# Kernel optimization log

Hardware: AMD Instinct MI355X
Metric: run time of the kernel (lower is better)

Reference implementation:

```python
import jax, jax.numpy as jnp
import numpy as np

N_HEADS, N_LEVELS, N_POINTS = 8, 3, 4


def _bilinear_sample(valf, Hl, Wl, grid):
    """torch.F.grid_sample(mode='bilinear', padding_mode='zeros', align_corners=False).
    valf: [B, nH, hd, Hl*Wl] flattened per-head value map
    grid: [B, Q, nH, P, 2] normalized (x, y) in [-1, 1]
    returns [B, nH, hd, Q, P]
    """
    B, Q, nH, P, _ = grid.shape
    hd = valf.shape[2]
    # unnormalize (align_corners=False)
    ix = ((grid[..., 0] + 1.0) * Wl - 1.0) * 0.5  # [B,Q,nH,P]
    iy = ((grid[..., 1] + 1.0) * Hl - 1.0) * 0.5
    x0 = jnp.floor(ix); y0 = jnp.floor(iy)
    x1 = x0 + 1.0;      y1 = y0 + 1.0
    # corner weights
    w00 = (x1 - ix) * (y1 - iy)
    w01 = (ix - x0) * (y1 - iy)
    w10 = (x1 - ix) * (iy - y0)
    w11 = (ix - x0) * (iy - y0)

    def gather(xi, yi):
        inb = (xi >= 0) & (xi <= Wl - 1) & (yi >= 0) & (yi <= Hl - 1)  # zero padding
        xc = jnp.clip(xi, 0, Wl - 1).astype(jnp.int32)
        yc = jnp.clip(yi, 0, Hl - 1).astype(jnp.int32)
        idx = yc * Wl + xc                              # [B,Q,nH,P]
        idx = idx.transpose(0, 2, 1, 3).reshape(B, nH, 1, Q * P)
        idx = jnp.broadcast_to(idx, (B, nH, hd, Q * P))
        g = jnp.take_along_axis(valf, idx, axis=3)      # [B,nH,hd,Q*P]
        g = g.reshape(B, nH, hd, Q, P)
        mask = inb.transpose(0, 2, 1, 3)[:, :, None, :, :]
        return g * mask

    def w_(w):  # [B,Q,nH,P] -> [B,nH,1,Q,P]
        return w.transpose(0, 2, 1, 3)[:, :, None, :, :]

    return (gather(x0, y0) * w_(w00) + gather(x1, y0) * w_(w01)
            + gather(x0, y1) * w_(w10) + gather(x1, y1) * w_(w11))


def _deform_attn(query, feats, reference_points,
                 W_off, b_off, W_attn, b_attn, W_val, b_val, W_out, b_out):
    B, Q, D = query.shape
    nH, L, P = N_HEADS, N_LEVELS, N_POINTS
    hd = D // nH
    # sampling offsets: tanh * 0.5
    off = jnp.tanh(query @ W_off + b_off).reshape(B, Q, nH, L, P, 2) * 0.5
    # attention weights: softmax over levels*points
    aw = jax.nn.softmax((query @ W_attn + b_attn).reshape(B, Q, nH, L * P), axis=-1)
    aw = aw.reshape(B, Q, nH, L, P)

    out = jnp.zeros((B, Q, nH, hd), dtype=query.dtype)
    for lvl, feat in enumerate(feats):
        Hl, Wl = feat.shape[2], feat.shape[3]
        # value projection on flattened map
        v = feat.reshape(B, D, Hl * Wl).transpose(0, 2, 1) @ W_val + b_val  # [B,S,D]
        valf = v.reshape(B, Hl * Wl, nH, hd).transpose(0, 2, 3, 1)          # [B,nH,hd,S]
        grid = (reference_points[:, :, None, None, :] + off[:, :, :, lvl]) * 2.0 - 1.0  # [B,Q,nH,P,2]
        sampled = _bilinear_sample(valf, Hl, Wl, grid)                      # [B,nH,hd,Q,P]
        w = aw[:, :, :, lvl].transpose(0, 2, 1, 3)[:, :, None, :, :]        # [B,nH,1,Q,P]
        out = out + (sampled * w).sum(-1).transpose(0, 3, 1, 2)             # [B,Q,nH,hd]
    return out.reshape(B, Q, D) @ W_out + b_out


def setup_inputs() -> dict:
    key = jax.random.key(0)
    ks = jax.random.split(key, 13)
    B, Q, D = 4, 8400, 256
    return {
        "query": jax.random.normal(ks[0], (B, Q, D), jnp.float32),
        "feat0": jax.random.normal(ks[1], (B, D, 80, 80), jnp.float32),
        "feat1": jax.random.normal(ks[2], (B, D, 40, 40), jnp.float32),
        "feat2": jax.random.normal(ks[3], (B, D, 20, 20), jnp.float32),
        "reference_points": jax.random.uniform(ks[4], (B, Q, 2), jnp.float32),
        "W_off": jax.random.normal(ks[5], (D, N_HEADS * N_LEVELS * N_POINTS * 2), jnp.float32) * 0.02,
        "b_off": jax.random.normal(ks[6], (N_HEADS * N_LEVELS * N_POINTS * 2,), jnp.float32) * 0.02,
        "W_attn": jax.random.normal(ks[7], (D, N_HEADS * N_LEVELS * N_POINTS), jnp.float32) * 0.02,
        "b_attn": jax.random.normal(ks[8], (N_HEADS * N_LEVELS * N_POINTS,), jnp.float32) * 0.02,
        "W_val": jax.random.normal(ks[9], (D, D), jnp.float32) * (1.0 / np.sqrt(D)),
        "b_val": jnp.zeros((D,), jnp.float32),
        "W_out": jax.random.normal(ks[10], (D, D), jnp.float32) * (1.0 / np.sqrt(D)),
        "b_out": jnp.zeros((D,), jnp.float32),
    }


def reference(query, feat0, feat1, feat2, reference_points,
              W_off, b_off, W_attn, b_attn, W_val, b_val, W_out, b_out):
    return _deform_attn(query, [feat0, feat1, feat2], reference_points,
                        W_off, b_off, W_attn, b_attn, W_val, b_val, W_out, b_out)
```

## Files before the change

kernel.cpp:

```cpp
#include <hip/hip_runtime.h>
#include <math.h>

#define NH    8
#define DIM   256
#define NQ    8400
#define BATCH 4
#define STOT  8400
#define MQ    (BATCH * NQ)

typedef _Float16 f16;
typedef __attribute__((ext_vector_type(2))) _Float16 f16x2;
typedef __attribute__((ext_vector_type(8))) _Float16 f16x8;
typedef __attribute__((ext_vector_type(8))) unsigned short u16x8;
typedef __attribute__((ext_vector_type(4))) float  f32x4;

static __device__ __forceinline__ void gl_lds16(const void* g, void* l) {
    __builtin_amdgcn_global_load_lds(
        (const __attribute__((address_space(1))) unsigned int*)g,
        (__attribute__((address_space(3))) unsigned int*)(unsigned int)(unsigned long long)l,
        16, 0, 0);
}

__global__ __launch_bounds__(256) void prep_all(
    const float* __restrict__ feat0, const float* __restrict__ feat1,
    const float* __restrict__ feat2, const float* __restrict__ query,
    const float* __restrict__ W_val, const float* __restrict__ W_out,
    const float* __restrict__ W_off, const float* __restrict__ W_attn,
    const float* __restrict__ b_off, const float* __restrict__ b_attn,
    f16* __restrict__ Af, f16* __restrict__ Qh,
    f16* __restrict__ Wvt, f16* __restrict__ Wot,
    f16* __restrict__ Wch, float* __restrict__ bcat)
{
    const int z = blockIdx.z;
    const int t = threadIdx.x;
    __shared__ float tile[32][33];
    const int c = t & 31, r = t >> 5;

    if (z == 5) {
        size_t base = ((size_t)(blockIdx.x * 8 + blockIdx.y) * 256 + t) * 16;
        if (base < (size_t)MQ * 256) {
            #pragma unroll
            for (int i = 0; i < 2; ++i) {
                float4 q0 = *(const float4*)(query + base + i * 8);
                float4 q1 = *(const float4*)(query + base + i * 8 + 4);
                f16x8 hv;
                hv[0] = (f16)q0.x; hv[1] = (f16)q0.y; hv[2] = (f16)q0.z; hv[3] = (f16)q0.w;
                hv[4] = (f16)q1.x; hv[5] = (f16)q1.y; hv[6] = (f16)q1.z; hv[7] = (f16)q1.w;
                *(f16x8*)(Qh + base + i * 8) = hv;
            }
        }
        return;
    }

    if (z == 4) {
        const int xb = blockIdx.x;
        if (xb > 25) return;
        if (xb == 25) {
            if (blockIdx.y == 0)
                for (int i = t; i < 288; i += 256)
                    bcat[i] = (i < 192) ? b_off[i] : b_attn[i - 192];
            return;
        }
        const float* W; f16* oH; int Nw, n0, nb;
        if (xb < 8)       { W = W_val;  oH = Wvt; Nw = 256; n0 = 0;   nb = xb * 32; }
        else if (xb < 16) { W = W_out;  oH = Wot; Nw = 256; n0 = 0;   nb = (xb - 8) * 32; }
        else if (xb < 22) { W = W_off;  oH = Wch; Nw = 192; n0 = 0;   nb = (xb - 16) * 32; }
        else              { W = W_attn; oH = Wch; Nw = 96;  n0 = 192; nb = (xb - 22) * 32; }
        const int k0 = blockIdx.y * 32;
        #pragma unroll
        for (int i = 0; i < 4; ++i) {
            int k = k0 + r + i * 8, n = nb + c;
            tile[r + i * 8][c] = (n < Nw) ? W[(size_t)k * Nw + n] : 0.f;
        }
        __syncthreads();
        #pragma unroll
        for (int i = 0; i < 4; ++i) {
            int n = nb + r + i * 8, k = k0 + c;
            if (n < Nw)
                oH[(size_t)(n0 + n) * 256 + k] = (f16)tile[c][r + i * 8];
        }
        return;
    }

    const int b = z;
    const int s0 = blockIdx.x * 32, k0 = blockIdx.y * 32;
    if (s0 >= 8400) return;
    const float* f0b = feat0 + (size_t)b * 256 * 6400;
    const float* f1b = feat1 + (size_t)b * 256 * 1600;
    const float* f2b = feat2 + (size_t)b * 256 * 400;
    #pragma unroll
    for (int i = 0; i < 4; ++i) {
        int rr = r + i * 8;
        int s = s0 + c;
        float v = 0.f;
        if (s < 8400) {
            const float* fp; int S, sl;
            if (s < 6400)      { fp = f0b; S = 6400; sl = s; }
            else if (s < 8000) { fp = f1b; S = 1600; sl = s - 6400; }
            else               { fp = f2b; S = 400;  sl = s - 8000; }
            v = fp[(size_t)(k0 + rr) * S + sl];
        }
        tile[rr][c] = v;
    }
    __syncthreads();
    #pragma unroll
    for (int i = 0; i < 4; ++i) {
        int s = s0 + r + i * 8, k = k0 + c;
        if (s < 8400)
            Af[((size_t)b * 8400 + s) * 256 + k] = (f16)tile[c][r + i * 8];
    }
}

template<int KIND>
__global__ __launch_bounds__(256) void gemm_glds(
    const f16* __restrict__ A0, const f16* __restrict__ A1,
    const f16* __restrict__ B0, const f16* __restrict__ B1,
    const float* __restrict__ bias0, const float* __restrict__ bias1,
    f16* __restrict__ valh, float* __restrict__ rawo, f16* __restrict__ attnh,
    float* __restrict__ Cf)
{
    __shared__ f16 Ah[128 * 32];
    __shared__ f16 Bs[128 * 32];

    const bool split = (KIND == 0) && (blockIdx.x >= 2);
    const int bn = split ? (blockIdx.x - 2) * 128 : blockIdx.x * 128;
    const int bm = blockIdx.y * 128;
    const int N = split ? 288 : 256;
    const f16* Ag = split ? A1 : A0;
    const f16* Bg = split ? B1 : B0;
    const float* bias = split ? bias1 : bias0;

    const int t = threadIdx.x;
    const int lane = t & 63, w = t >> 6;
    const int wm = (w & 1) * 64, wn = (w >> 1) * 64;
    const int l15 = lane & 15, quad = lane >> 4;

    const int fstage = ((t >> 2) & 3) ^ ((t >> 4) & 3);
    const int qs = (t & 3) ^ fstage;
    const int ffrag = (l15 & 3) ^ ((l15 >> 2) & 3);
    const int qf = quad ^ ffrag;

    f32x4 acc[4][4];
    #pragma unroll
    for (int i = 0; i < 4; ++i)
        #pragma unroll
        for (int j = 0; j < 4; ++j)
            acc[i][j] = (f32x4){0.f, 0.f, 0.f, 0.f};

    for (int k0 = 0; k0 < 256; k0 += 32) {
        #pragma unroll
        for (int i = 0; i < 2; ++i) {
            int row = i * 64 + (t >> 2);
            int slot = i * 256 + t;
            int gr = bm + row; if (gr > MQ - 1) gr = MQ - 1;
            gl_lds16(Ag + (size_t)gr * 256 + k0 + qs * 8, &Ah[slot * 8]);
            int gn = bn + row; if (gn > N - 1) gn = N - 1;
            gl_lds16(Bg + (size_t)gn * 256 + k0 + qs * 8, &Bs[slot * 8]);
        }
        __syncthreads();

        f16x8 af[4], bfv[4];
        #pragma unroll
        for (int mt = 0; mt < 4; ++mt)
            af[mt] = *(const f16x8*)&Ah[((wm + mt * 16 + l15) * 4 + qf) * 8];
        #pragma unroll
        for (int nt = 0; nt < 4; ++nt)
            bfv[nt] = *(const f16x8*)&Bs[((wn + nt * 16 + l15) * 4 + qf) * 8];
        #pragma unroll
        for (int mt = 0; mt < 4; ++mt)
            #pragma unroll
            for (int nt = 0; nt < 4; ++nt)
                acc[mt][nt] = __builtin_amdgcn_mfma_f32_16x16x32_f16(af[mt], bfv[nt], acc[mt][nt], 0, 0, 0);
        __syncthreads();
    }

    #pragma unroll
    for (int nt = 0; nt < 4; ++nt) {
        int col = bn + wn + nt * 16 + l15;
        float bv = (col < N) ? bias[col] : 0.f;
        #pragma unroll
        for (int mt = 0; mt < 4; ++mt) {
            int row0 = bm + wm + mt * 16 + quad * 4;
            #pragma unroll
            for (int r = 0; r < 4; ++r) {
                int row = row0 + r;
                if (row >= MQ || col >= N) continue;
                float v = acc[mt][nt][r] + bv;
                if (KIND == 1) {
                    Cf[(size_t)row * 256 + col] = v;
                } else if (!split) {
                    int bb = row / STOT, s = row - bb * STOT;
                    int h = col >> 5, c = col & 31;
                    valh[(((size_t)(bb * 8 + h)) * STOT + s) * 32 + c] = (f16)v;
                } else if (col < 192) {
                    rawo[(size_t)row * 192 + col] = v;
                } else {
                    attnh[(size_t)row * 96 + (col - 192)] = (f16)v;
                }
            }
        }
    }
}

__global__ __launch_bounds__(256) void sample_v6(
    const f16* __restrict__ valh,
    const float* __restrict__ raw_off,
    const f16* __restrict__ attnh,
    const float* __restrict__ refp,
    f16* __restrict__ out_h)
{
    const int bx = blockIdx.x;
    const int xcd = bx & 7;
    const int b = xcd >> 1;
    const int qi = (bx >> 3) * 2 + (xcd & 1);
    const int bq0 = b * NQ + qi * 8;
    const int t = threadIdx.x;

    __shared__ int      s_idx[8][96][4];
    __shared__ unsigned s_wp[8][96][4];
    __shared__ float    s_m[8][8];
    __shared__ float    s_inv[8][8];

    if (t < 64) {
        int q = t >> 3, h = t & 7;
        const f16* a = attnh + (size_t)(bq0 + q) * 96 + h * 12;
        float m = (float)a[0];
        #pragma unroll
        for (int j = 1; j < 12; ++j) m = fmaxf(m, (float)a[j]);
        float s = 0.f;
        #pragma unroll
        for (int j = 0; j < 12; ++j) s += expf((float)a[j] - m);
        s_m[q][h] = m;
        s_inv[q][h] = 1.f / s;
    }
    __syncthreads();

    for (int i = t; i < 768; i += 256) {
        int q = i / 96, p = i - q * 96;
        int h = p / 12, lp = p - h * 12, l = lp >> 2;
        const int dims[3]   = {80, 40, 20};
        const int bases_[3] = {0, 6400, 8000};
        int Wl = dims[l], base = bases_[l];
        float logit = (float)attnh[(size_t)(bq0 + q) * 96 + p];
        float aw = expf(logit - s_m[q][h]) * s_inv[q][h];
        size_t ro = (size_t)(bq0 + q) * 192 + h * 24 + lp * 2;
        float rawx = raw_off[ro], rawy = raw_off[ro + 1];
        float rx = refp[(size_t)(bq0 + q) * 2];
        float ry = refp[(size_t)(bq0 + q) * 2 + 1];
        float ix = (rx + tanhf(rawx) * 0.5f) * Wl - 0.5f;
        float iy = (ry + tanhf(rawy) * 0.5f) * Wl - 0.5f;
        float x0f = floorf(ix), y0f = floorf(iy);
        float fx = ix - x0f, fy = iy - y0f;
        int x0 = (int)x0f, y0 = (int)y0f;
        float w00 = (1.f - fx) * (1.f - fy) * aw;
        float w01 = fx * (1.f - fy) * aw;
        float w10 = (1.f - fx) * fy * aw;
        float w11 = fx * fy * aw;
        bool vx0 = (unsigned)x0 < (unsigned)Wl;
        bool vx1 = (unsigned)(x0 + 1) < (unsigned)Wl;
        bool vy0 = (unsigned)y0 < (unsigned)Wl;
        bool vy1 = (unsigned)(y0 + 1) < (unsigned)Wl;
        int row0 = base + y0 * Wl, row1 = row0 + Wl;
        float ws[4] = { vx0 && vy0 ? w00 : 0.f, vx1 && vy0 ? w01 : 0.f,
                        vx0 && vy1 ? w10 : 0.f, vx1 && vy1 ? w11 : 0.f };
        int   is[4] = { vx0 && vy0 ? row0 + x0 : 0, vx1 && vy0 ? row0 + x0 + 1 : 0,
                        vx0 && vy1 ? row1 + x0 : 0, vx1 && vy1 ? row1 + x0 + 1 : 0 };
        #pragma unroll
        for (int k = 0; k < 4; ++k) {
            unsigned short us = __builtin_bit_cast(unsigned short, (f16)ws[k]);
            s_wp[q][p][k] = ((unsigned)us << 16) | us;
            s_idx[q][p][k] = is[k];
        }
    }
    __syncthreads();

    const int q = t >> 5;
    const int h = (t >> 2) & 7;
    const int l4 = t & 3;
    const uint4* vb4 = (const uint4*)(valh + (size_t)(b * 8 + h) * STOT * 32);
    const int*      ip = &s_idx[q][h * 12][0];
    const unsigned* wp = &s_wp[q][h * 12][0];
    float accf[8] = {};
    #pragma unroll
    for (int pp = 0; pp < 4; ++pp) {
        int ix[12]; unsigned ww[12]; uint4 v[12];
        #pragma unroll
        for (int k = 0; k < 12; ++k) { ix[k] = ip[pp * 12 + k]; ww[k] = wp[pp * 12 + k]; }
        #pragma unroll
        for (int k = 0; k < 12; ++k) v[k] = vb4[(size_t)ix[k] * 4 + l4];
        f16x2 a0 = (f16x2)(f16)0, a1 = a0, a2 = a0, a3 = a0;
        #pragma unroll
        for (int k = 0; k < 12; ++k) {
            f16x2 wv = __builtin_bit_cast(f16x2, ww[k]);
            a0 += wv * __builtin_bit_cast(f16x2, v[k].x);
            a1 += wv * __builtin_bit_cast(f16x2, v[k].y);
            a2 += wv * __builtin_bit_cast(f16x2, v[k].z);
            a3 += wv * __builtin_bit_cast(f16x2, v[k].w);
        }
        accf[0] += (float)a0[0]; accf[1] += (float)a0[1];
        accf[2] += (float)a1[0]; accf[3] += (float)a1[1];
        accf[4] += (float)a2[0]; accf[5] += (float)a2[1];
        accf[6] += (float)a3[0]; accf[7] += (float)a3[1];
    }
    f16x8 ob;
    #pragma unroll
    for (int c = 0; c < 8; ++c) ob[c] = (f16)accf[c];
    *(f16x8*)(out_h + (size_t)(bq0 + q) * 256 + h * 32 + l4 * 8) = ob;
}

extern "C" void kernel_launch(void* const* d_in, const int* in_sizes, int n_in,
                              void* d_out, int out_size, void* d_ws, size_t ws_size,
                              hipStream_t stream)
{
    const float* query  = (const float*)d_in[0];
    const float* feat0  = (const float*)d_in[1];
    const float* feat1  = (const float*)d_in[2];
    const float* feat2  = (const float*)d_in[3];
    const float* refp   = (const float*)d_in[4];
    const float* W_off  = (const float*)d_in[5];
    const float* b_off  = (const float*)d_in[6];
    const float* W_attn = (const float*)d_in[7];
    const float* b_attn = (const float*)d_in[8];
    const float* W_val  = (const float*)d_in[9];
    const float* b_val  = (const float*)d_in[10];
    const float* W_out  = (const float*)d_in[11];
    const float* b_out  = (const float*)d_in[12];
    float* out = (float*)d_out;

    f16*   valh  = (f16*)d_ws;
    float* rawo  = (float*)(valh + (size_t)MQ * 256);
    f16*   attnh = (f16*)(rawo + (size_t)MQ * 192);
    f16*   Af    = attnh + (size_t)MQ * 96;
    f16*   outh  = Af;
    f16*   Qh    = Af + (size_t)MQ * 256;
    f16*   Wvt   = Qh + (size_t)MQ * 256;
    f16*   Wot   = Wvt + 65536;
    f16*   Wch   = Wot + 65536;
    float* bcat  = (float*)(Wch + 73728);

    dim3 blk(256);

    prep_all<<<dim3(263, 8, 6), blk, 0, stream>>>(feat0, feat1, feat2, query,
                                                  W_val, W_out, W_off, W_attn,
                                                  b_off, b_attn,
                                                  Af, Qh, Wvt, Wot, Wch, bcat);
    gemm_glds<0><<<dim3(5, 263), blk, 0, stream>>>(Af, Qh, Wvt, Wch, b_val, bcat,
                                                   valh, rawo, attnh, nullptr);
    sample_v6<<<dim3(MQ / 8), blk, 0, stream>>>(valh, rawo, attnh, refp, outh);
    gemm_glds<1><<<dim3(2, 263), blk, 0, stream>>>(outh, nullptr, Wot, nullptr,
                                                   b_out, nullptr,
                                                   nullptr, nullptr, nullptr, out);
}
```

Baseline: 239.8 us.

## Fuse fp32-to-fp16 feature/query conversion into GEMM A-tile loads, move tanh to epilogue

The separate prep pass that transposed feature maps and converted the query to fp16 is removed. The first GEMM now reads fp32 features (strided by spatial size) and fp32 query directly, converting to fp16 while staging into a padded LDS tile. This avoids writing and re-reading two large fp16 intermediates. The offset tanh*0.5 moves into the GEMM epilogue, and the sampler packs index and weight into one LDS word. The risk is strided, poorly coalesced feature loads through registers instead of async global-to-LDS copies. The packed word also truncates the sample index to 16 bits.

```diff
diff --git a/kernel.cpp b/kernel.cpp
--- a/kernel.cpp
+++ b/kernel.cpp
@@ -11,7 +11,6 @@
 typedef _Float16 f16;
 typedef __attribute__((ext_vector_type(2))) _Float16 f16x2;
 typedef __attribute__((ext_vector_type(8))) _Float16 f16x8;
-typedef __attribute__((ext_vector_type(8))) unsigned short u16x8;
 typedef __attribute__((ext_vector_type(4))) float  f32x4;
 
 static __device__ __forceinline__ void gl_lds16(const void* g, void* l) {
@@ -21,112 +20,61 @@
         16, 0, 0);
 }
 
-__global__ __launch_bounds__(256) void prep_all(
-    const float* __restrict__ feat0, const float* __restrict__ feat1,
-    const float* __restrict__ feat2, const float* __restrict__ query,
+__global__ __launch_bounds__(256) void prep_w(
     const float* __restrict__ W_val, const float* __restrict__ W_out,
     const float* __restrict__ W_off, const float* __restrict__ W_attn,
     const float* __restrict__ b_off, const float* __restrict__ b_attn,
-    f16* __restrict__ Af, f16* __restrict__ Qh,
-    f16* __restrict__ Wvt, f16* __restrict__ Wot,
-    f16* __restrict__ Wch, float* __restrict__ bcat)
+    f16* __restrict__ Wvt, f16* __restrict__ Wot, f16* __restrict__ Wch,
+    float* __restrict__ bcat)
 {
-    const int z = blockIdx.z;
+    const int xb = blockIdx.x;
     const int t = threadIdx.x;
     __shared__ float tile[32][33];
     const int c = t & 31, r = t >> 5;
 
-    if (z == 5) {
-        size_t base = ((size_t)(blockIdx.x * 8 + blockIdx.y) * 256 + t) * 16;
-        if (base < (size_t)MQ * 256) {
-            #pragma unroll
-            for (int i = 0; i < 2; ++i) {
-                float4 q0 = *(const float4*)(query + base + i * 8);
-                float4 q1 = *(const float4*)(query + base + i * 8 + 4);
-                f16x8 hv;
-                hv[0] = (f16)q0.x; hv[1] = (f16)q0.y; hv[2] = (f16)q0.z; hv[3] = (f16)q0.w;
-                hv[4] = (f16)q1.x; hv[5] = (f16)q1.y; hv[6] = (f16)q1.z; hv[7] = (f16)q1.w;
-                *(f16x8*)(Qh + base + i * 8) = hv;
-            }
-        }
+    if (xb == 25) {
+        if (blockIdx.y == 0)
+            for (int i = t; i < 288; i += 256)
+                bcat[i] = (i < 192) ? b_off[i] : b_attn[i - 192];
         return;
     }
-
-    if (z == 4) {
-        const int xb = blockIdx.x;
-        if (xb > 25) return;
-        if (xb == 25) {
-            if (blockIdx.y == 0)
-                for (int i = t; i < 288; i += 256)
-                    bcat[i] = (i < 192) ? b_off[i] : b_attn[i - 192];
-            return;
-        }
-        const float* W; f16* oH; int Nw, n0, nb;
-        if (xb < 8)       { W = W_val;  oH = Wvt; Nw = 256; n0 = 0;   nb = xb * 32; }
-        else if (xb < 16) { W = W_out;  oH = Wot; Nw = 256; n0 = 0;   nb = (xb - 8) * 32; }
-        else if (xb < 22) { W = W_off;  oH = Wch; Nw = 192; n0 = 0;   nb = (xb - 16) * 32; }
-        else              { W = W_attn; oH = Wch; Nw = 96;  n0 = 192; nb = (xb - 22) * 32; }
-        const int k0 = blockIdx.y * 32;
-        #pragma unroll
-        for (int i = 0; i < 4; ++i) {
-            int k = k0 + r + i * 8, n = nb + c;
-            tile[r + i * 8][c] = (n < Nw) ? W[(size_t)k * Nw + n] : 0.f;
-        }
-        __syncthreads();
-        #pragma unroll
-        for (int i = 0; i < 4; ++i) {
-            int n = nb + r + i * 8, k = k0 + c;
-            if (n < Nw)
-                oH[(size_t)(n0 + n) * 256 + k] = (f16)tile[c][r + i * 8];
-        }
-        return;
-    }
-
-    const int b = z;
-    const int s0 = blockIdx.x * 32, k0 = blockIdx.y * 32;
-    if (s0 >= 8400) return;
-    const float* f0b = feat0 + (size_t)b * 256 * 6400;
-    const float* f1b = feat1 + (size_t)b * 256 * 1600;
-    const float* f2b = feat2 + (size_t)b * 256 * 400;
+    const float* W; f16* oH; int Nw, n0, nb;
+    if (xb < 8)       { W = W_val;  oH = Wvt; Nw = 256; n0 = 0;   nb = xb * 32; }
+    else if (xb < 16) { W = W_out;  oH = Wot; Nw = 256; n0 = 0;   nb = (xb - 8) * 32; }
+    else if (xb < 22) { W = W_off;  oH = Wch; Nw = 192; n0 = 0;   nb = (xb - 16) * 32; }
+    else              { W = W_attn; oH = Wch; Nw = 96;  n0 = 192; nb = (xb - 22) * 32; }
+    const int k0 = blockIdx.y * 32;
     #pragma unroll
     for (int i = 0; i < 4; ++i) {
-        int rr = r + i * 8;
-        int s = s0 + c;
-        float v = 0.f;
-        if (s < 8400) {
-            const float* fp; int S, sl;
-            if (s < 6400)      { fp = f0b; S = 6400; sl = s; }
-            else if (s < 8000) { fp = f1b; S = 1600; sl = s - 6400; }
-            else               { fp = f2b; S = 400;  sl = s - 8000; }
-            v = fp[(size_t)(k0 + rr) * S + sl];
-        }
-        tile[rr][c] = v;
+        int k = k0 + r + i * 8, n = nb + c;
+        tile[r + i * 8][c] = (n < Nw) ? W[(size_t)k * Nw + n] : 0.f;
     }
     __syncthreads();
     #pragma unroll
     for (int i = 0; i < 4; ++i) {
-        int s = s0 + r + i * 8, k = k0 + c;
-        if (s < 8400)
-            Af[((size_t)b * 8400 + s) * 256 + k] = (f16)tile[c][r + i * 8];
+        int n = nb + r + i * 8, k = k0 + c;
+        if (n < Nw)
+            oH[(size_t)(n0 + n) * 256 + k] = (f16)tile[c][r + i * 8];
     }
 }
 
 template<int KIND>
-__global__ __launch_bounds__(256) void gemm_glds(
-    const f16* __restrict__ A0, const f16* __restrict__ A1,
+__global__ __launch_bounds__(256) void gemm_fused(
+    const float* __restrict__ feat0, const float* __restrict__ feat1,
+    const float* __restrict__ feat2, const float* __restrict__ query,
+    const f16* __restrict__ A16,
     const f16* __restrict__ B0, const f16* __restrict__ B1,
     const float* __restrict__ bias0, const float* __restrict__ bias1,
     f16* __restrict__ valh, float* __restrict__ rawo, f16* __restrict__ attnh,
     float* __restrict__ Cf)
 {
-    __shared__ f16 Ah[128 * 32];
-    __shared__ f16 Bs[128 * 32];
+    __shared__ __align__(16) f16 Ahs[128 * 40];
+    __shared__ __align__(16) f16 Bs[128 * 32];
 
     const bool split = (KIND == 0) && (blockIdx.x >= 2);
     const int bn = split ? (blockIdx.x - 2) * 128 : blockIdx.x * 128;
     const int bm = blockIdx.y * 128;
     const int N = split ? 288 : 256;
-    const f16* Ag = split ? A1 : A0;
     const f16* Bg = split ? B1 : B0;
     const float* bias = split ? bias1 : bias0;
 
@@ -140,6 +88,20 @@
     const int ffrag = (l15 & 3) ^ ((l15 >> 2) & 3);
     const int qf = quad ^ ffrag;
 
+    const float* aptr = nullptr; int Sv = 0;
+    int rA0 = 0, kqA = 0;
+    if (KIND == 0 && !split) {
+        const int spair = t >> 2;
+        kqA = t & 3;
+        rA0 = spair * 2;
+        int gr = bm + rA0;
+        if (gr + 1 >= MQ) gr = MQ - 2;
+        int bb = gr / STOT, s = gr - bb * STOT;
+        if (s < 6400)      { aptr = feat0 + (size_t)bb * 256 * 6400 + s;          Sv = 6400; }
+        else if (s < 8000) { aptr = feat1 + (size_t)bb * 256 * 1600 + (s - 6400); Sv = 1600; }
+        else               { aptr = feat2 + (size_t)bb * 256 * 400  + (s - 8000); Sv = 400;  }
+    }
+
     f32x4 acc[4][4];
     #pragma unroll
     for (int i = 0; i < 4; ++i)
@@ -148,12 +110,40 @@
             acc[i][j] = (f32x4){0.f, 0.f, 0.f, 0.f};
 
     for (int k0 = 0; k0 < 256; k0 += 32) {
+        if (KIND == 0 && !split) {
+            float2 va[8];
+            #pragma unroll
+            for (int j = 0; j < 8; ++j)
+                va[j] = *(const float2*)(aptr + (size_t)(k0 + kqA * 8 + j) * Sv);
+            f16x8 h0, h1;
+            #pragma unroll
+            for (int j = 0; j < 8; ++j) { h0[j] = (f16)va[j].x; h1[j] = (f16)va[j].y; }
+            *(f16x8*)&Ahs[((rA0)     * 5 + kqA) * 8] = h0;
+            *(f16x8*)&Ahs[((rA0 + 1) * 5 + kqA) * 8] = h1;
+        } else if (KIND == 0) {
+            #pragma unroll
+            for (int i = 0; i < 2; ++i) {
+                int row = i * 64 + (t >> 2), q4 = t & 3;
+                int gr = bm + row; if (gr > MQ - 1) gr = MQ - 1;
+                const float* qp = query + (size_t)gr * 256 + k0 + q4 * 8;
+                float4 a = *(const float4*)qp;
+                float4 b = *(const float4*)(qp + 4);
+                f16x8 h;
+                h[0] = (f16)a.x; h[1] = (f16)a.y; h[2] = (f16)a.z; h[3] = (f16)a.w;
+                h[4] = (f16)b.x; h[5] = (f16)b.y; h[6] = (f16)b.z; h[7] = (f16)b.w;
+                *(f16x8*)&Ahs[(row * 5 + q4) * 8] = h;
+            }
+        } else {
+            #pragma unroll
+            for (int i = 0; i < 2; ++i) {
+                int row = i * 64 + (t >> 2), slot = i * 256 + t;
+                int gr = bm + row; if (gr > MQ - 1) gr = MQ - 1;
+                gl_lds16(A16 + (size_t)gr * 256 + k0 + qs * 8, &Ahs[slot * 8]);
+            }
+        }
         #pragma unroll
         for (int i = 0; i < 2; ++i) {
-            int row = i * 64 + (t >> 2);
-            int slot = i * 256 + t;
-            int gr = bm + row; if (gr > MQ - 1) gr = MQ - 1;
-            gl_lds16(Ag + (size_t)gr * 256 + k0 + qs * 8, &Ah[slot * 8]);
+            int row = i * 64 + (t >> 2), slot = i * 256 + t;
             int gn = bn + row; if (gn > N - 1) gn = N - 1;
             gl_lds16(Bg + (size_t)gn * 256 + k0 + qs * 8, &Bs[slot * 8]);
         }
@@ -161,8 +151,12 @@
 
         f16x8 af[4], bfv[4];
         #pragma unroll
-        for (int mt = 0; mt < 4; ++mt)
-            af[mt] = *(const f16x8*)&Ah[((wm + mt * 16 + l15) * 4 + qf) * 8];
+        for (int mt = 0; mt < 4; ++mt) {
+            int ar = wm + mt * 16 + l15;
+            af[mt] = (KIND == 0)
+                ? *(const f16x8*)&Ahs[(ar * 5 + quad) * 8]
+                : *(const f16x8*)&Ahs[(ar * 4 + qf) * 8];
+        }
         #pragma unroll
         for (int nt = 0; nt < 4; ++nt)
             bfv[nt] = *(const f16x8*)&Bs[((wn + nt * 16 + l15) * 4 + qf) * 8];
@@ -193,7 +187,7 @@
                     int h = col >> 5, c = col & 31;
                     valh[(((size_t)(bb * 8 + h)) * STOT + s) * 32 + c] = (f16)v;
                 } else if (col < 192) {
-                    rawo[(size_t)row * 192 + col] = v;
+                    rawo[(size_t)row * 192 + col] = 0.5f * tanhf(v);
                 } else {
                     attnh[(size_t)row * 96 + (col - 192)] = (f16)v;
                 }
@@ -202,9 +196,9 @@
     }
 }
 
-__global__ __launch_bounds__(256) void sample_v6(
+__global__ __launch_bounds__(256) void sample_v7(
     const f16* __restrict__ valh,
-    const float* __restrict__ raw_off,
+    const float* __restrict__ off05,
     const f16* __restrict__ attnh,
     const float* __restrict__ refp,
     f16* __restrict__ out_h)
@@ -216,8 +210,7 @@
     const int bq0 = b * NQ + qi * 8;
     const int t = threadIdx.x;
 
-    __shared__ int      s_idx[8][96][4];
-    __shared__ unsigned s_wp[8][96][4];
+    __shared__ unsigned s_pk[8][96][4];
     __shared__ float    s_m[8][8];
     __shared__ float    s_inv[8][8];
 
@@ -244,11 +237,11 @@
         float logit = (float)attnh[(size_t)(bq0 + q) * 96 + p];
         float aw = expf(logit - s_m[q][h]) * s_inv[q][h];
         size_t ro = (size_t)(bq0 + q) * 192 + h * 24 + lp * 2;
-        float rawx = raw_off[ro], rawy = raw_off[ro + 1];
+        float ox = off05[ro], oy = off05[ro + 1];
         float rx = refp[(size_t)(bq0 + q) * 2];
         float ry = refp[(size_t)(bq0 + q) * 2 + 1];
-        float ix = (rx + tanhf(rawx) * 0.5f) * Wl - 0.5f;
-        float iy = (ry + tanhf(rawy) * 0.5f) * Wl - 0.5f;
+        float ix = (rx + ox) * Wl - 0.5f;
+        float iy = (ry + oy) * Wl - 0.5f;
         float x0f = floorf(ix), y0f = floorf(iy);
         float fx = ix - x0f, fy = iy - y0f;
         int x0 = (int)x0f, y0 = (int)y0f;
@@ -268,8 +261,7 @@
         #pragma unroll
         for (int k = 0; k < 4; ++k) {
             unsigned short us = __builtin_bit_cast(unsigned short, (f16)ws[k]);
-            s_wp[q][p][k] = ((unsigned)us << 16) | us;
-            s_idx[q][p][k] = is[k];
+            s_pk[q][p][k] = ((unsigned)us << 16) | (unsigned)is[k];
         }
     }
     __syncthreads();
@@ -278,20 +270,20 @@
     const int h = (t >> 2) & 7;
     const int l4 = t & 3;
     const uint4* vb4 = (const uint4*)(valh + (size_t)(b * 8 + h) * STOT * 32);
-    const int*      ip = &s_idx[q][h * 12][0];
-    const unsigned* wp = &s_wp[q][h * 12][0];
+    const unsigned* pkp = &s_pk[q][h * 12][0];
     float accf[8] = {};
     #pragma unroll
     for (int pp = 0; pp < 4; ++pp) {
-        int ix[12]; unsigned ww[12]; uint4 v[12];
-        #pragma unroll
-        for (int k = 0; k < 12; ++k) { ix[k] = ip[pp * 12 + k]; ww[k] = wp[pp * 12 + k]; }
-        #pragma unroll
-        for (int k = 0; k < 12; ++k) v[k] = vb4[(size_t)ix[k] * 4 + l4];
+        unsigned pk[12]; uint4 v[12];
+        #pragma unroll
+        for (int k = 0; k < 12; ++k) pk[k] = pkp[pp * 12 + k];
+        #pragma unroll
+        for (int k = 0; k < 12; ++k) v[k] = vb4[(size_t)(pk[k] & 0xffffu) * 4 + l4];
         f16x2 a0 = (f16x2)(f16)0, a1 = a0, a2 = a0, a3 = a0;
         #pragma unroll
         for (int k = 0; k < 12; ++k) {
-            f16x2 wv = __builtin_bit_cast(f16x2, ww[k]);
+            f16x2 wv = __builtin_bit_cast(f16x2,
+                        __builtin_amdgcn_perm(pk[k], pk[k], 0x03020302u));
             a0 += wv * __builtin_bit_cast(f16x2, v[k].x);
             a1 += wv * __builtin_bit_cast(f16x2, v[k].y);
             a2 += wv * __builtin_bit_cast(f16x2, v[k].z);
@@ -330,24 +322,21 @@
     f16*   valh  = (f16*)d_ws;
     float* rawo  = (float*)(valh + (size_t)MQ * 256);
     f16*   attnh = (f16*)(rawo + (size_t)MQ * 192);
-    f16*   Af    = attnh + (size_t)MQ * 96;
-    f16*   outh  = Af;
-    f16*   Qh    = Af + (size_t)MQ * 256;
-    f16*   Wvt   = Qh + (size_t)MQ * 256;
+    f16*   outh  = attnh + (size_t)MQ * 96;
+    f16*   Wvt   = outh + (size_t)MQ * 256;
     f16*   Wot   = Wvt + 65536;
     f16*   Wch   = Wot + 65536;
     float* bcat  = (float*)(Wch + 73728);
 
     dim3 blk(256);
 
-    prep_all<<<dim3(263, 8, 6), blk, 0, stream>>>(feat0, feat1, feat2, query,
-                                                  W_val, W_out, W_off, W_attn,
-                                                  b_off, b_attn,
-                                                  Af, Qh, Wvt, Wot, Wch, bcat);
-    gemm_glds<0><<<dim3(5, 263), blk, 0, stream>>>(Af, Qh, Wvt, Wch, b_val, bcat,
-                                                   valh, rawo, attnh, nullptr);
-    sample_v6<<<dim3(MQ / 8), blk, 0, stream>>>(valh, rawo, attnh, refp, outh);
-    gemm_glds<1><<<dim3(2, 263), blk, 0, stream>>>(outh, nullptr, Wot, nullptr,
-                                                   b_out, nullptr,
-                                                   nullptr, nullptr, nullptr, out);
-}
+    prep_w<<<dim3(26, 8), blk, 0, stream>>>(W_val, W_out, W_off, W_attn,
+                                            b_off, b_attn, Wvt, Wot, Wch, bcat);
+    gemm_fused<0><<<dim3(5, 263), blk, 0, stream>>>(feat0, feat1, feat2, query, nullptr,
+                                                    Wvt, Wch, b_val, bcat,
+                                                    valh, rawo, attnh, nullptr);
+    sample_v7<<<dim3(MQ / 8), blk, 0, stream>>>(valh, rawo, attnh, refp, outh);
+    gemm_fused<1><<<dim3(2, 263), blk, 0, stream>>>(feat0, feat1, feat2, query, outh,
+                                                    Wot, nullptr, b_out, nullptr,
+                                                    nullptr, nullptr, nullptr, out);
+}
```

After: 257.2 us. 7.2% more time.

## Restructure GEMMs with LDS-resident full-K B tiles and fused query conversion

Applied to the files above, without the earlier changes.

The GEMM kernel is rewritten so each block loads the whole 64-column by 256-K weight tile into swizzled LDS once, and keeps A fragments in registers read straight from global memory. This removes the per-K-step barrier loop. The query fp32-to-fp16 conversion pass moves out of the prep kernel and into the GEMM A-load, which avoids writing and re-reading a half-precision query buffer. The tanh on sampling offsets moves into the GEMM epilogue. The sampler packs index and weight into one 32-bit LDS word, which halves its shared-memory traffic. The cost is more register pressure, a 32KB LDS tile per block, and more blocks along N.

```diff
diff --git a/kernel.cpp b/kernel.cpp
--- a/kernel.cpp
+++ b/kernel.cpp
@@ -11,7 +11,6 @@
 typedef _Float16 f16;
 typedef __attribute__((ext_vector_type(2))) _Float16 f16x2;
 typedef __attribute__((ext_vector_type(8))) _Float16 f16x8;
-typedef __attribute__((ext_vector_type(8))) unsigned short u16x8;
 typedef __attribute__((ext_vector_type(4))) float  f32x4;
 
 static __device__ __forceinline__ void gl_lds16(const void* g, void* l) {
@@ -21,36 +20,19 @@
         16, 0, 0);
 }
 
-__global__ __launch_bounds__(256) void prep_all(
+__global__ __launch_bounds__(256) void prep_feat(
     const float* __restrict__ feat0, const float* __restrict__ feat1,
-    const float* __restrict__ feat2, const float* __restrict__ query,
+    const float* __restrict__ feat2,
     const float* __restrict__ W_val, const float* __restrict__ W_out,
     const float* __restrict__ W_off, const float* __restrict__ W_attn,
     const float* __restrict__ b_off, const float* __restrict__ b_attn,
-    f16* __restrict__ Af, f16* __restrict__ Qh,
-    f16* __restrict__ Wvt, f16* __restrict__ Wot,
+    f16* __restrict__ Af, f16* __restrict__ Wvt, f16* __restrict__ Wot,
     f16* __restrict__ Wch, float* __restrict__ bcat)
 {
     const int z = blockIdx.z;
     const int t = threadIdx.x;
     __shared__ float tile[32][33];
     const int c = t & 31, r = t >> 5;
-
-    if (z == 5) {
-        size_t base = ((size_t)(blockIdx.x * 8 + blockIdx.y) * 256 + t) * 16;
-        if (base < (size_t)MQ * 256) {
-            #pragma unroll
-            for (int i = 0; i < 2; ++i) {
-                float4 q0 = *(const float4*)(query + base + i * 8);
-                float4 q1 = *(const float4*)(query + base + i * 8 + 4);
-                f16x8 hv;
-                hv[0] = (f16)q0.x; hv[1] = (f16)q0.y; hv[2] = (f16)q0.z; hv[3] = (f16)q0.w;
-                hv[4] = (f16)q1.x; hv[5] = (f16)q1.y; hv[6] = (f16)q1.z; hv[7] = (f16)q1.w;
-                *(f16x8*)(Qh + base + i * 8) = hv;
-            }
-        }
-        return;
-    }
 
     if (z == 4) {
         const int xb = blockIdx.x;
@@ -112,75 +94,101 @@
 }
 
 template<int KIND>
-__global__ __launch_bounds__(256) void gemm_glds(
-    const f16* __restrict__ A0, const f16* __restrict__ A1,
-    const f16* __restrict__ B0, const f16* __restrict__ B1,
-    const float* __restrict__ bias0, const float* __restrict__ bias1,
+__global__ __launch_bounds__(256) void gemm_bs(
+    const float* __restrict__ query,
+    const f16* __restrict__ Af,
+    const f16* __restrict__ outh_in,
+    const f16* __restrict__ Wvt, const f16* __restrict__ Wch,
+    const f16* __restrict__ Wot,
+    const float* __restrict__ b_val, const float* __restrict__ bcat,
+    const float* __restrict__ b_out,
     f16* __restrict__ valh, float* __restrict__ rawo, f16* __restrict__ attnh,
     float* __restrict__ Cf)
 {
-    __shared__ f16 Ah[128 * 32];
-    __shared__ f16 Bs[128 * 32];
-
-    const bool split = (KIND == 0) && (blockIdx.x >= 2);
-    const int bn = split ? (blockIdx.x - 2) * 128 : blockIdx.x * 128;
-    const int bm = blockIdx.y * 128;
-    const int N = split ? 288 : 256;
-    const f16* Ag = split ? A1 : A0;
-    const f16* Bg = split ? B1 : B0;
-    const float* bias = split ? bias1 : bias0;
+    __shared__ __align__(16) f16 Bsl[2048 * 8];
 
     const int t = threadIdx.x;
     const int lane = t & 63, w = t >> 6;
-    const int wm = (w & 1) * 64, wn = (w >> 1) * 64;
     const int l15 = lane & 15, quad = lane >> 4;
 
-    const int fstage = ((t >> 2) & 3) ^ ((t >> 4) & 3);
-    const int qs = (t & 3) ^ fstage;
-    const int ffrag = (l15 & 3) ^ ((l15 >> 2) & 3);
-    const int qf = quad ^ ffrag;
-
-    f32x4 acc[4][4];
-    #pragma unroll
-    for (int i = 0; i < 4; ++i)
+    const bool qpath = (KIND == 0) && (blockIdx.x >= 4);
+    const int bn = qpath ? (blockIdx.x - 4) * 64 : blockIdx.x * 64;
+    const int bm = blockIdx.y * 128;
+    const int N  = qpath ? 288 : 256;
+    const f16* Bg = (KIND == 0) ? (qpath ? Wch : Wvt) : Wot;
+    const float* bias = (KIND == 0) ? (qpath ? bcat : b_val) : b_out;
+
+    #pragma unroll
+    for (int i = 0; i < 8; ++i) {
+        int slot = i * 256 + t;
+        int n = slot >> 5, cp = slot & 31;
+        int cc = cp ^ (n & 7);
+        int gn = bn + n; if (gn > N - 1) gn = N - 1;
+        gl_lds16(Bg + (size_t)gn * 256 + cc * 8, &Bsl[slot * 8]);
+    }
+
+    const int r0 = bm + w * 32 + l15;
+    f16x8 areg[2][8];
+    if (KIND == 0 && qpath) {
+        #pragma unroll
+        for (int mt = 0; mt < 2; ++mt) {
+            int row = r0 + mt * 16; if (row > MQ - 1) row = MQ - 1;
+            const float* ap = query + (size_t)row * 256 + quad * 8;
+            #pragma unroll
+            for (int kt = 0; kt < 8; ++kt) {
+                float4 a = *(const float4*)(ap + kt * 32);
+                float4 b = *(const float4*)(ap + kt * 32 + 4);
+                f16x8 h;
+                h[0] = (f16)a.x; h[1] = (f16)a.y; h[2] = (f16)a.z; h[3] = (f16)a.w;
+                h[4] = (f16)b.x; h[5] = (f16)b.y; h[6] = (f16)b.z; h[7] = (f16)b.w;
+                areg[mt][kt] = h;
+            }
+        }
+    } else {
+        const f16* Ag = (KIND == 0) ? Af : outh_in;
+        #pragma unroll
+        for (int mt = 0; mt < 2; ++mt) {
+            int row = r0 + mt * 16; if (row > MQ - 1) row = MQ - 1;
+            const f16* ap = Ag + (size_t)row * 256 + quad * 8;
+            #pragma unroll
+            for (int kt = 0; kt < 8; ++kt)
+                areg[mt][kt] = *(const f16x8*)(ap + kt * 32);
+        }
+    }
+
+    f32x4 acc[2][4];
+    #pragma unroll
+    for (int i = 0; i < 2; ++i)
         #pragma unroll
         for (int j = 0; j < 4; ++j)
             acc[i][j] = (f32x4){0.f, 0.f, 0.f, 0.f};
 
-    for (int k0 = 0; k0 < 256; k0 += 32) {
-        #pragma unroll
-        for (int i = 0; i < 2; ++i) {
-            int row = i * 64 + (t >> 2);
-            int slot = i * 256 + t;
-            int gr = bm + row; if (gr > MQ - 1) gr = MQ - 1;
-            gl_lds16(Ag + (size_t)gr * 256 + k0 + qs * 8, &Ah[slot * 8]);
-            int gn = bn + row; if (gn > N - 1) gn = N - 1;
-            gl_lds16(Bg + (size_t)gn * 256 + k0 + qs * 8, &Bs[slot * 8]);
-        }
-        __syncthreads();
-
-        f16x8 af[4], bfv[4];
-        #pragma unroll
-        for (int mt = 0; mt < 4; ++mt)
-            af[mt] = *(const f16x8*)&Ah[((wm + mt * 16 + l15) * 4 + qf) * 8];
-        #pragma unroll
-        for (int nt = 0; nt < 4; ++nt)
-            bfv[nt] = *(const f16x8*)&Bs[((wn + nt * 16 + l15) * 4 + qf) * 8];
-        #pragma unroll
-        for (int mt = 0; mt < 4; ++mt)
+    __syncthreads();
+
+    #pragma unroll
+    for (int kt = 0; kt < 8; ++kt) {
+        f16x8 bfv[4];
+        #pragma unroll
+        for (int nt = 0; nt < 4; ++nt) {
+            int n = nt * 16 + l15;
+            int cp = (kt * 4 + quad) ^ (n & 7);
+            bfv[nt] = *(const f16x8*)&Bsl[((size_t)n * 32 + cp) * 8];
+        }
+        #pragma unroll
+        for (int mt = 0; mt < 2; ++mt)
             #pragma unroll
             for (int nt = 0; nt < 4; ++nt)
-                acc[mt][nt] = __builtin_amdgcn_mfma_f32_16x16x32_f16(af[mt], bfv[nt], acc[mt][nt], 0, 0, 0);
-        __syncthreads();
+                acc[mt][nt] = __builtin_amdgcn_mfma_f32_16x16x32_f16(
+                                  areg[mt][kt], bfv[nt], acc[mt][nt], 0, 0, 0);
     }
 
     #pragma unroll
     for (int nt = 0; nt < 4; ++nt) {
-        int col = bn + wn + nt * 16 + l15;
+        int col = bn + nt * 16 + l15;
         float bv = (col < N) ? bias[col] : 0.f;
         #pragma unroll
-        for (int mt = 0; mt < 4; ++mt) {
-            int row0 = bm + wm + mt * 16 + quad * 4;
+        for (int mt = 0; mt < 2; ++mt) {
+            int row0 = bm + w * 32 + mt * 16 + quad * 4;
             #pragma unroll
             for (int r = 0; r < 4; ++r) {
                 int row = row0 + r;
@@ -188,12 +196,12 @@
                 float v = acc[mt][nt][r] + bv;
                 if (KIND == 1) {
                     Cf[(size_t)row * 256 + col] = v;
-                } else if (!split) {
+                } else if (!qpath) {
                     int bb = row / STOT, s = row - bb * STOT;
                     int h = col >> 5, c = col & 31;
                     valh[(((size_t)(bb * 8 + h)) * STOT + s) * 32 + c] = (f16)v;
                 } else if (col < 192) {
-                    rawo[(size_t)row * 192 + col] = v;
+                    rawo[(size_t)row * 192 + col] = 0.5f * tanhf(v);
                 } else {
                     attnh[(size_t)row * 96 + (col - 192)] = (f16)v;
                 }
@@ -202,9 +210,9 @@
     }
 }
 
-__global__ __launch_bounds__(256) void sample_v6(
+__global__ __launch_bounds__(256) void sample_v7(
     const f16* __restrict__ valh,
-    const float* __restrict__ raw_off,
+    const float* __restrict__ off05,
     const f16* __restrict__ attnh,
     const float* __restrict__ refp,
     f16* __restrict__ out_h)
@@ -216,8 +224,7 @@
     const int bq0 = b * NQ + qi * 8;
     const int t = threadIdx.x;
 
-    __shared__ int      s_idx[8][96][4];
-    __shared__ unsigned s_wp[8][96][4];
+    __shared__ unsigned s_pk[8][96][4];
     __shared__ float    s_m[8][8];
     __shared__ float    s_inv[8][8];
 
@@ -244,11 +251,11 @@
         float logit = (float)attnh[(size_t)(bq0 + q) * 96 + p];
         float aw = expf(logit - s_m[q][h]) * s_inv[q][h];
         size_t ro = (size_t)(bq0 + q) * 192 + h * 24 + lp * 2;
-        float rawx = raw_off[ro], rawy = raw_off[ro + 1];
+        float ox = off05[ro], oy = off05[ro + 1];
         float rx = refp[(size_t)(bq0 + q) * 2];
         float ry = refp[(size_t)(bq0 + q) * 2 + 1];
-        float ix = (rx + tanhf(rawx) * 0.5f) * Wl - 0.5f;
-        float iy = (ry + tanhf(rawy) * 0.5f) * Wl - 0.5f;
+        float ix = (rx + ox) * Wl - 0.5f;
+        float iy = (ry + oy) * Wl - 0.5f;
         float x0f = floorf(ix), y0f = floorf(iy);
         float fx = ix - x0f, fy = iy - y0f;
         int x0 = (int)x0f, y0 = (int)y0f;
@@ -268,8 +275,7 @@
         #pragma unroll
         for (int k = 0; k < 4; ++k) {
             unsigned short us = __builtin_bit_cast(unsigned short, (f16)ws[k]);
-            s_wp[q][p][k] = ((unsigned)us << 16) | us;
-            s_idx[q][p][k] = is[k];
+            s_pk[q][p][k] = ((unsigned)us << 16) | (unsigned)is[k];
         }
     }
     __syncthreads();
@@ -278,20 +284,20 @@
     const int h = (t >> 2) & 7;
     const int l4 = t & 3;
     const uint4* vb4 = (const uint4*)(valh + (size_t)(b * 8 + h) * STOT * 32);
-    const int*      ip = &s_idx[q][h * 12][0];
-    const unsigned* wp = &s_wp[q][h * 12][0];
+    const unsigned* pkp = &s_pk[q][h * 12][0];
     float accf[8] = {};
     #pragma unroll
     for (int pp = 0; pp < 4; ++pp) {
-        int ix[12]; unsigned ww[12]; uint4 v[12];
-        #pragma unroll
-        for (int k = 0; k < 12; ++k) { ix[k] = ip[pp * 12 + k]; ww[k] = wp[pp * 12 + k]; }
-        #pragma unroll
-        for (int k = 0; k < 12; ++k) v[k] = vb4[(size_t)ix[k] * 4 + l4];
+        unsigned pk[12]; uint4 v[12];
+        #pragma unroll
+        for (int k = 0; k < 12; ++k) pk[k] = pkp[pp * 12 + k];
+        #pragma unroll
+        for (int k = 0; k < 12; ++k) v[k] = vb4[(size_t)(pk[k] & 0xffffu) * 4 + l4];
         f16x2 a0 = (f16x2)(f16)0, a1 = a0, a2 = a0, a3 = a0;
         #pragma unroll
         for (int k = 0; k < 12; ++k) {
-            f16x2 wv = __builtin_bit_cast(f16x2, ww[k]);
+            f16x2 wv = __builtin_bit_cast(f16x2,
+                        __builtin_amdgcn_perm(pk[k], pk[k], 0x03020302u));
             a0 += wv * __builtin_bit_cast(f16x2, v[k].x);
             a1 += wv * __builtin_bit_cast(f16x2, v[k].y);
             a2 += wv * __builtin_bit_cast(f16x2, v[k].z);
@@ -332,22 +338,22 @@
     f16*   attnh = (f16*)(rawo + (size_t)MQ * 192);
     f16*   Af    = attnh + (size_t)MQ * 96;
     f16*   outh  = Af;
-    f16*   Qh    = Af + (size_t)MQ * 256;
-    f16*   Wvt   = Qh + (size_t)MQ * 256;
+    f16*   Wvt   = Af + (size_t)MQ * 256;
     f16*   Wot   = Wvt + 65536;
     f16*   Wch   = Wot + 65536;
     float* bcat  = (float*)(Wch + 73728);
 
     dim3 blk(256);
 
-    prep_all<<<dim3(263, 8, 6), blk, 0, stream>>>(feat0, feat1, feat2, query,
-                                                  W_val, W_out, W_off, W_attn,
-                                                  b_off, b_attn,
-                                                  Af, Qh, Wvt, Wot, Wch, bcat);
-    gemm_glds<0><<<dim3(5, 263), blk, 0, stream>>>(Af, Qh, Wvt, Wch, b_val, bcat,
-                                                   valh, rawo, attnh, nullptr);
-    sample_v6<<<dim3(MQ / 8), blk, 0, stream>>>(valh, rawo, attnh, refp, outh);
-    gemm_glds<1><<<dim3(2, 263), blk, 0, stream>>>(outh, nullptr, Wot, nullptr,
-                                                   b_out, nullptr,
-                                                   nullptr, nullptr, nullptr, out);
-}
+    prep_feat<<<dim3(263, 8, 5), blk, 0, stream>>>(feat0, feat1, feat2,
+                                                   W_val, W_out, W_off, W_attn,
+                                                   b_off, b_attn,
+                                                   Af, Wvt, Wot, Wch, bcat);
+    gemm_bs<0><<<dim3(9, 263), blk, 0, stream>>>(query, Af, nullptr,
+                                                 Wvt, Wch, Wot, b_val, bcat, b_out,
+                                                 valh, rawo, attnh, nullptr);
+    sample_v7<<<dim3(MQ / 8), blk, 0, stream>>>(valh, rawo, attnh, refp, outh);
+    gemm_bs<1><<<dim3(4, 263), blk, 0, stream>>>(query, Af, outh,
+                                                 Wvt, Wch, Wot, b_val, bcat, b_out,
+                                                 nullptr, nullptr, nullptr, out);
+}
```

Result: slower. 259.1 us (+8.0%).
